# Performance work log

Measured on AMD Instinct MI355X. Metric: run time of the kernel, lower is better.

The kernel has to match this reference:

```python
import jax, jax.numpy as jnp
import numpy as np

N_NODES = 100000
N_EDGES = 1000000
IN_DIM = 64
OUT_DIM = 64
BN_EPS = 1e-5


def setup_inputs() -> dict:
    key = jax.random.key(0)
    k1, k2, k3 = jax.random.split(key, 3)
    x = jax.random.normal(k1, (N_NODES, IN_DIM), dtype=jnp.float32)
    edge_index = jax.random.randint(k2, (2, N_EDGES), 0, N_NODES, dtype=jnp.int32)
    W = jax.random.normal(k3, (IN_DIM, OUT_DIM), dtype=jnp.float32) * (1.0 / np.sqrt(IN_DIM))
    b = jnp.zeros((OUT_DIM,), dtype=jnp.float32)
    gamma = jnp.ones((OUT_DIM,), dtype=jnp.float32)
    beta = jnp.zeros((OUT_DIM,), dtype=jnp.float32)
    return {"x": x, "edge_index": edge_index, "W": W, "b": b, "gamma": gamma, "beta": beta}


def reference(x, edge_index, W, b, gamma, beta):
    N = x.shape[0]
    # GCN normalization with self-loops (improved=False -> fill value 1.0)
    loop = jnp.arange(N, dtype=edge_index.dtype)
    src = jnp.concatenate([edge_index[0], loop])  # message sources
    dst = jnp.concatenate([edge_index[1], loop])  # aggregation targets
    ew = jnp.ones(src.shape[0], dtype=x.dtype)
    deg = jax.ops.segment_sum(ew, dst, num_segments=N)  # [N]
    dinv = jnp.where(deg > 0, jax.lax.rsqrt(deg), 0.0)
    norm = dinv[src] * ew * dinv[dst]  # [E+N]
    # linear transform then normalized scatter-add aggregation
    h = x @ W  # [N, OUT_DIM]
    msg = h[src] * norm[:, None]  # [E+N, OUT_DIM]
    agg = jax.ops.segment_sum(msg, dst, num_segments=N) + b  # [N, OUT_DIM]
    # activation
    a = jax.nn.relu(agg)
    # BatchNorm1d, training mode: batch statistics over node dim (biased var)
    mean = jnp.mean(a, axis=0)
    var = jnp.mean((a - mean) ** 2, axis=0)
    out = gamma * (a - mean) * jax.lax.rsqrt(var + BN_EPS) + beta
    return out
```

## Files before the change

kernel.cpp:

```cpp
#include <hip/hip_runtime.h>
#include <hip/hip_fp16.h>

#define DIM 64
#define BN_EPS 1e-5f
#define RSHIFT 8
#define RSIZE 256
#define EPB 2048
#define ABLK 2048
#define RBLK 128
#define BH 512

__global__ __launch_bounds__(256) void k_binhist(const int* __restrict__ dst,
                                                 int* __restrict__ bhist,
                                                 int P, int E) {
    __shared__ int hist[BH];
    for (int b0 = threadIdx.x; b0 < BH; b0 += 256) hist[b0] = 0;
    __syncthreads();
    const int base4 = blockIdx.x * (EPB / 4);
    for (int i = 0; i < EPB / 4 / 256; ++i) {
        int idx = base4 + i * 256 + threadIdx.x;
        int e0 = idx << 2;
        if (e0 + 3 < E) {
            int4 d4 = ((const int4*)dst)[idx];
            atomicAdd(&hist[d4.x >> RSHIFT], 1);
            atomicAdd(&hist[d4.y >> RSHIFT], 1);
            atomicAdd(&hist[d4.z >> RSHIFT], 1);
            atomicAdd(&hist[d4.w >> RSHIFT], 1);
        } else {
            for (int k = 0; k < 4; ++k)
                if (e0 + k < E) atomicAdd(&hist[dst[e0 + k] >> RSHIFT], 1);
        }
    }
    __syncthreads();
    for (int b0 = threadIdx.x; b0 < P; b0 += 256)
        bhist[blockIdx.x * BH + b0] = hist[b0];
}

__global__ __launch_bounds__(128) void k_binscan(int* __restrict__ bhist,
                                                 int* __restrict__ bintot,
                                                 int nbin) {
    __shared__ int s[128];
    const int r = blockIdx.x;
    int carry = 0;
    for (int base = 0; base < nbin; base += 128) {
        const int idx = base + threadIdx.x;
        int v = (idx < nbin) ? bhist[idx * BH + r] : 0;
        s[threadIdx.x] = v;
        __syncthreads();
        for (int off = 1; off < 128; off <<= 1) {
            int t = (threadIdx.x >= (unsigned)off) ? s[threadIdx.x - off] : 0;
            __syncthreads();
            s[threadIdx.x] += t;
            __syncthreads();
        }
        if (idx < nbin) bhist[idx * BH + r] = carry + s[threadIdx.x] - v;
        carry += s[127];
        __syncthreads();
    }
    if (threadIdx.x == 0) bintot[r] = carry;
}

__global__ void k_gscan(const int* __restrict__ bintot, int* __restrict__ gbase,
                        int* __restrict__ rowptr, int P, int N, int E) {
    __shared__ int s[512];
    int v = ((int)threadIdx.x < P) ? bintot[threadIdx.x] : 0;
    s[threadIdx.x] = v;
    __syncthreads();
    for (int off = 1; off < 512; off <<= 1) {
        int t = (threadIdx.x >= (unsigned)off) ? s[threadIdx.x - off] : 0;
        __syncthreads();
        s[threadIdx.x] += t;
        __syncthreads();
    }
    if ((int)threadIdx.x < P) gbase[threadIdx.x] = s[threadIdx.x] - v;
    if ((int)threadIdx.x == P - 1) gbase[P] = s[threadIdx.x];
    if (threadIdx.x == 0) rowptr[N] = E;
}

__global__ __launch_bounds__(256) void k_bin(const int* __restrict__ src,
                                             const int* __restrict__ dst,
                                             const int* __restrict__ gbase,
                                             const int* __restrict__ bhist,
                                             int* __restrict__ pk, int P, int E) {
    __shared__ int gofs[BH], lcnt[BH];
    for (int b0 = threadIdx.x; b0 < P; b0 += 256) {
        gofs[b0] = gbase[b0] + bhist[blockIdx.x * BH + b0];
        lcnt[b0] = 0;
    }
    __syncthreads();
    const int base4 = blockIdx.x * (EPB / 4);
    for (int i = 0; i < EPB / 4 / 256; ++i) {
        int idx = base4 + i * 256 + threadIdx.x;
        int e0 = idx << 2;
        if (e0 + 3 < E) {
            int4 d4 = ((const int4*)dst)[idx];
            int4 s4 = ((const int4*)src)[idx];
            int b0;
            b0 = d4.x >> RSHIFT; pk[gofs[b0] + atomicAdd(&lcnt[b0], 1)] = ((d4.x & (RSIZE - 1)) << 20) | s4.x;
            b0 = d4.y >> RSHIFT; pk[gofs[b0] + atomicAdd(&lcnt[b0], 1)] = ((d4.y & (RSIZE - 1)) << 20) | s4.y;
            b0 = d4.z >> RSHIFT; pk[gofs[b0] + atomicAdd(&lcnt[b0], 1)] = ((d4.z & (RSIZE - 1)) << 20) | s4.z;
            b0 = d4.w >> RSHIFT; pk[gofs[b0] + atomicAdd(&lcnt[b0], 1)] = ((d4.w & (RSIZE - 1)) << 20) | s4.w;
        } else {
            for (int k = 0; k < 4; ++k) {
                if (e0 + k < E) {
                    int d = dst[e0 + k];
                    int b0 = d >> RSHIFT;
                    pk[gofs[b0] + atomicAdd(&lcnt[b0], 1)] = ((d & (RSIZE - 1)) << 20) | src[e0 + k];
                }
            }
        }
    }
}

__global__ __launch_bounds__(512) void k_sortrange(
        const int* __restrict__ gbase, const int* __restrict__ pk,
        int* __restrict__ ssrc, int* __restrict__ rowptr,
        float* __restrict__ dinv, int N) {
    __shared__ int lhist[256], ls[256], lcur[256];
    const int r = blockIdx.x;
    const int d0 = r << RSHIFT;
    const int tid = threadIdx.x;
    const int i = d0 + tid;
    const int ebeg = gbase[r], eend = gbase[r + 1];
    if (tid < 256) lhist[tid] = 0;
    __syncthreads();
    for (int j = ebeg + tid; j < eend; j += 512)
        atomicAdd(&lhist[((unsigned)pk[j]) >> 20], 1);
    __syncthreads();
    int dg = 0;
    if (tid < 256) {
        dg = lhist[tid];
        if (i < N) dinv[i] = rsqrtf((float)dg + 1.0f);
        ls[tid] = dg;
    }
    __syncthreads();
    for (int off = 1; off < 256; off <<= 1) {
        int t = (tid < 256 && tid >= off) ? ls[tid - off] : 0;
        __syncthreads();
        if (tid < 256) ls[tid] += t;
        __syncthreads();
    }
    if (tid < 256) {
        int lofs = ls[tid] - dg;
        lcur[tid] = ebeg + lofs;
        if (i < N) rowptr[i] = ebeg + lofs;
    }
    __syncthreads();
    for (int j = ebeg + tid; j < eend; j += 512) {
        int p = pk[j];
        ssrc[atomicAdd(&lcur[((unsigned)p) >> 20], 1)] = p & 0xFFFFF;
    }
}

__global__ __launch_bounds__(256) void k_gemm(const float* __restrict__ x,
                                              const float* __restrict__ W,
                                              const float* __restrict__ dinv,
                                              __half* __restrict__ h2, int N) {
    __shared__ float Wl[DIM * DIM];
    for (int i = threadIdx.x; i < DIM * DIM; i += 256) Wl[i] = W[i];
    __syncthreads();
    int t = blockIdx.x * 256 + threadIdx.x;
    int r = t >> 2;
    int q = t & 3;
    if (r >= N) return;
    const float4* xr4 = (const float4*)(x + (size_t)r * DIM);
    float4 acc[4];
#pragma unroll
    for (int j = 0; j < 4; ++j) acc[j] = make_float4(0.f, 0.f, 0.f, 0.f);
    for (int k0 = 0; k0 < 16; ++k0) {
        float4 xv = xr4[k0];
#pragma unroll
        for (int kk = 0; kk < 4; ++kk) {
            float xs = (&xv.x)[kk];
            const float4* wrow = (const float4*)(Wl + (k0 * 4 + kk) * DIM) + (q << 2);
#pragma unroll
            for (int j = 0; j < 4; ++j) {
                float4 w = wrow[j];
                acc[j].x += xs * w.x;
                acc[j].y += xs * w.y;
                acc[j].z += xs * w.z;
                acc[j].w += xs * w.w;
            }
        }
    }
    float dr = dinv[r];
    float4* hr4 = (float4*)(h2 + (size_t)r * DIM) + (q << 1);
    union { __half2 h[4]; float4 f4; } pack;
#pragma unroll
    for (int j = 0; j < 4; j += 2) {
        pack.h[0] = __float22half2_rn(make_float2(acc[j].x * dr, acc[j].y * dr));
        pack.h[1] = __float22half2_rn(make_float2(acc[j].z * dr, acc[j].w * dr));
        pack.h[2] = __float22half2_rn(make_float2(acc[j + 1].x * dr, acc[j + 1].y * dr));
        pack.h[3] = __float22half2_rn(make_float2(acc[j + 1].z * dr, acc[j + 1].w * dr));
        hr4[j >> 1] = pack.f4;
    }
}

#define GATHER_BATCH(B)                                                             \
    {                                                                               \
        int sA[B]; float vA[B];                                                     \
        _Pragma("unroll")                                                           \
        for (int k = 0; k < B; ++k) sA[k] = __builtin_amdgcn_readlane(sv, j + k);   \
        _Pragma("unroll")                                                           \
        for (int k = 0; k < B; ++k) vA[k] = __half2float(hb[(size_t)sA[k] * DIM]);  \
        _Pragma("unroll")                                                           \
        for (int k = 0; k < B; ++k) {                                               \
            if (j + k < c) acc0 += vA[k]; else acc1 += vA[k];                       \
        }                                                                           \
        j += B;                                                                     \
    }

__global__ __launch_bounds__(256) void k_nodeagg(
        const int* __restrict__ rowptr, const int* __restrict__ ssrc,
        const __half* __restrict__ h2, const float* __restrict__ dinv,
        const float* __restrict__ b, __half* __restrict__ a2,
        float* __restrict__ pstats, int N) {
    const int lane = threadIdx.x & 63;
    const int w = threadIdx.x >> 6;
    const float bl = b[lane];
    const __half* hb = h2 + lane;
    float psum = 0.f, psq = 0.f;
    const int npairs = N >> 1;
    for (int t = blockIdx.x * 4 + w; t < npairs; t += ABLK * 4) {
        const int i0 = t << 1;
        const int rb0 = rowptr[i0], rb1 = rowptr[i0 + 1], rb2 = rowptr[i0 + 2];
        float acc0 = __half2float(hb[(size_t)i0 * DIM]);
        float acc1 = __half2float(hb[(size_t)(i0 + 1) * DIM]);
        const int total = rb2 - rb0;
        for (int j0 = 0; j0 < total; j0 += 64) {
            const int m = min(64, total - j0);
            const int c = rb1 - rb0 - j0;
            int sv = ssrc[rb0 + j0 + min(lane, m - 1)];
            int j = 0;
            while (j + 16 <= m) GATHER_BATCH(16)
            if (j + 8 <= m) GATHER_BATCH(8)
            if (j + 4 <= m) GATHER_BATCH(4)
            for (; j < m; ++j) {
                int sj = __builtin_amdgcn_readlane(sv, j);
                float v = __half2float(hb[(size_t)sj * DIM]);
                if (j < c) acc0 += v; else acc1 += v;
            }
        }
        float a0 = fmaxf(acc0 * dinv[i0] + bl, 0.f);
        float a1 = fmaxf(acc1 * dinv[i0 + 1] + bl, 0.f);
        a2[(size_t)i0 * DIM + lane] = __float2half_rn(a0);
        a2[(size_t)(i0 + 1) * DIM + lane] = __float2half_rn(a1);
        psum += a0 + a1;
        psq += a0 * a0 + a1 * a1;
    }
    __shared__ float s1[256], s2[256];
    s1[threadIdx.x] = psum;
    s2[threadIdx.x] = psq;
    __syncthreads();
    if (threadIdx.x < 128) {
        s1[threadIdx.x] += s1[threadIdx.x + 128];
        s2[threadIdx.x] += s2[threadIdx.x + 128];
    }
    __syncthreads();
    if (threadIdx.x < 64) {
        pstats[(size_t)blockIdx.x * 128 + threadIdx.x] = s1[threadIdx.x] + s1[threadIdx.x + 64];
        pstats[(size_t)blockIdx.x * 128 + 64 + threadIdx.x] = s2[threadIdx.x] + s2[threadIdx.x + 64];
    }
}

__global__ __launch_bounds__(128) void k_redstats(const float* __restrict__ pstats,
                                                  float* __restrict__ pstats2) {
    const int f = threadIdx.x;
    const size_t base = (size_t)blockIdx.x * (ABLK / RBLK) * 128;
    float s = 0.f;
#pragma unroll 8
    for (int j = 0; j < ABLK / RBLK; ++j)
        s += pstats[base + (size_t)j * 128 + f];
    pstats2[(size_t)blockIdx.x * 128 + f] = s;
}

__global__ void k_finstats(const float* __restrict__ pstats2,
                           const float* __restrict__ gamma, const float* __restrict__ beta,
                           float* __restrict__ scale, float* __restrict__ shift, int N) {
    __shared__ float ssum[1024], ssq[1024];
    const int f = threadIdx.x & 63;
    const int c = threadIdx.x >> 6;
    float s = 0.f, q = 0.f;
    for (int blk = c; blk < RBLK; blk += 16) {
        s += pstats2[blk * 128 + f];
        q += pstats2[blk * 128 + 64 + f];
    }
    ssum[threadIdx.x] = s;
    ssq[threadIdx.x] = q;
    __syncthreads();
    for (int o = 512; o >= 64; o >>= 1) {
        if ((int)threadIdx.x < o) {
            ssum[threadIdx.x] += ssum[threadIdx.x + o];
            ssq[threadIdx.x] += ssq[threadIdx.x + o];
        }
        __syncthreads();
    }
    if (threadIdx.x < 64) {
        float inv_n = 1.0f / (float)N;
        float mean = ssum[f] * inv_n;
        float var = ssq[f] * inv_n - mean * mean;
        float istd = rsqrtf(var + BN_EPS);
        float sc = gamma[f] * istd;
        scale[f] = sc;
        shift[f] = beta[f] - mean * sc;
    }
}

__global__ void k_bn2(const __half* __restrict__ a2, const float* __restrict__ scale,
                      const float* __restrict__ shift, float* __restrict__ out, int total8) {
    int i = blockIdx.x * blockDim.x + threadIdx.x;
    const int stride = gridDim.x * blockDim.x;
    const int f8 = i & 7;
    const float4 sc0 = ((const float4*)scale)[f8 * 2];
    const float4 sc1 = ((const float4*)scale)[f8 * 2 + 1];
    const float4 sh0 = ((const float4*)shift)[f8 * 2];
    const float4 sh1 = ((const float4*)shift)[f8 * 2 + 1];
    for (; i < total8; i += stride) {
        union { float4 f; __half2 h[4]; } u;
        u.f = ((const float4*)a2)[i];
        float2 p0 = __half22float2(u.h[0]);
        float2 p1 = __half22float2(u.h[1]);
        float2 p2 = __half22float2(u.h[2]);
        float2 p3 = __half22float2(u.h[3]);
        float4 o0 = make_float4(p0.x * sc0.x + sh0.x, p0.y * sc0.y + sh0.y,
                                p1.x * sc0.z + sh0.z, p1.y * sc0.w + sh0.w);
        float4 o1 = make_float4(p2.x * sc1.x + sh1.x, p2.y * sc1.y + sh1.y,
                                p3.x * sc1.z + sh1.z, p3.y * sc1.w + sh1.w);
        ((float4*)out)[(size_t)i * 2] = o0;
        ((float4*)out)[(size_t)i * 2 + 1] = o1;
    }
}

extern "C" void kernel_launch(void* const* d_in, const int* in_sizes, int n_in,
                              void* d_out, int out_size, void* d_ws, size_t ws_size,
                              hipStream_t stream) {
    const float* x     = (const float*)d_in[0];
    const int*   ei    = (const int*)d_in[1];
    const float* W     = (const float*)d_in[2];
    const float* b     = (const float*)d_in[3];
    const float* gamma = (const float*)d_in[4];
    const float* beta  = (const float*)d_in[5];
    float* out = (float*)d_out;

    const int N = in_sizes[0] / DIM;
    const int E = in_sizes[1] / 2;
    const int* esrc = ei;
    const int* edst = ei + E;
    const int P = (N + RSIZE - 1) >> RSHIFT;
    const int nbin = (E + EPB - 1) / EPB;

    char* ws = (char*)d_ws;
    size_t off = 0;
    int* bhist = (int*)(ws + off);      off += (size_t)nbin * BH * sizeof(int);
    off = (off + 255) & ~(size_t)255;
    int* bintot = (int*)(ws + off);     off += 512 * sizeof(int);
    int* gbase = (int*)(ws + off);      off += 520 * sizeof(int);
    off = (off + 255) & ~(size_t)255;
    float* dinv = (float*)(ws + off);   off += (size_t)N * sizeof(float);
    off = (off + 255) & ~(size_t)255;
    int* rowptr = (int*)(ws + off);     off += (size_t)(N + 1) * sizeof(int);
    off = (off + 255) & ~(size_t)255;
    float* scale = (float*)(ws + off);  off += 64 * sizeof(float);
    float* shift = (float*)(ws + off);  off += 64 * sizeof(float);
    off = (off + 255) & ~(size_t)255;
    float* pstats = (float*)(ws + off); off += (size_t)ABLK * 128 * sizeof(float);
    off = (off + 255) & ~(size_t)255;
    float* pstats2 = (float*)(ws + off); off += (size_t)RBLK * 128 * sizeof(float);
    off = (off + 255) & ~(size_t)255;
    int* pk = (int*)(ws + off);         off += (size_t)E * sizeof(int);
    off = (off + 255) & ~(size_t)255;
    int* ssrc = (int*)(ws + off);       off += (size_t)E * sizeof(int);
    off = (off + 255) & ~(size_t)255;
    __half* h2 = (__half*)(ws + off);   off += (size_t)N * DIM * sizeof(__half);
    off = (off + 255) & ~(size_t)255;
    __half* a2 = (__half*)(ws + off);   off += (size_t)N * DIM * sizeof(__half);

    k_binhist<<<nbin, 256, 0, stream>>>(edst, bhist, P, E);
    k_binscan<<<P, 128, 0, stream>>>(bhist, bintot, nbin);
    k_gscan<<<1, 512, 0, stream>>>(bintot, gbase, rowptr, P, N, E);
    k_bin<<<nbin, 256, 0, stream>>>(esrc, edst, gbase, bhist, pk, P, E);
    k_sortrange<<<P, 512, 0, stream>>>(gbase, pk, ssrc, rowptr, dinv, N);
    k_gemm<<<(4 * N + 255) / 256, 256, 0, stream>>>(x, W, dinv, h2, N);
    k_nodeagg<<<ABLK, 256, 0, stream>>>(rowptr, ssrc, h2, dinv, b, a2, pstats, N);
    k_redstats<<<RBLK, 128, 0, stream>>>(pstats, pstats2);
    k_finstats<<<1, 1024, 0, stream>>>(pstats2, gamma, beta, scale, shift, N);
    k_bn2<<<1024, 256, 0, stream>>>(a2, scale, shift, out, N * DIM / 8);
}
```

Baseline: 181.5 us.

## Fuse histogram and binning into one pass with block-local bucketed output

The two-pass global bucket sort (histogram, scan, then scatter) becomes a single kernel in which each block histograms its 2048 edges, scans locally, and writes packed entries grouped by bucket into its own slice of the pk buffer. Per-block offsets and counts are packed into one metadata word. The binscan is replaced by a plain reduction, and sortrange now walks every block's segment for its bucket. This drops one full read of the edge arrays and one kernel launch. In exchange, sortrange does irregular, serial per-thread loops over many small segments (about 489 blocks per bucket, with only a few entries each), which may load-balance and coalesce poorly.

```diff
diff --git a/kernel.cpp b/kernel.cpp
--- a/kernel.cpp
+++ b/kernel.cpp
@@ -10,54 +10,64 @@
 #define RBLK 128
 #define BH 512
 
-__global__ __launch_bounds__(256) void k_binhist(const int* __restrict__ dst,
-                                                 int* __restrict__ bhist,
-                                                 int P, int E) {
-    __shared__ int hist[BH];
-    for (int b0 = threadIdx.x; b0 < BH; b0 += 256) hist[b0] = 0;
-    __syncthreads();
-    const int base4 = blockIdx.x * (EPB / 4);
-    for (int i = 0; i < EPB / 4 / 256; ++i) {
-        int idx = base4 + i * 256 + threadIdx.x;
-        int e0 = idx << 2;
-        if (e0 + 3 < E) {
-            int4 d4 = ((const int4*)dst)[idx];
-            atomicAdd(&hist[d4.x >> RSHIFT], 1);
-            atomicAdd(&hist[d4.y >> RSHIFT], 1);
-            atomicAdd(&hist[d4.z >> RSHIFT], 1);
-            atomicAdd(&hist[d4.w >> RSHIFT], 1);
-        } else {
-            for (int k = 0; k < 4; ++k)
-                if (e0 + k < E) atomicAdd(&hist[dst[e0 + k] >> RSHIFT], 1);
-        }
-    }
-    __syncthreads();
-    for (int b0 = threadIdx.x; b0 < P; b0 += 256)
-        bhist[blockIdx.x * BH + b0] = hist[b0];
-}
-
-__global__ __launch_bounds__(128) void k_binscan(int* __restrict__ bhist,
-                                                 int* __restrict__ bintot,
-                                                 int nbin) {
+__global__ __launch_bounds__(512) void k_bin2(const int* __restrict__ src,
+                                              const int* __restrict__ dst,
+                                              int* __restrict__ meta,
+                                              int* __restrict__ pk, int P, int E) {
+    __shared__ int hist[BH], ls[BH], lcur[BH];
+    const int tid = threadIdx.x;
+    hist[tid] = 0;
+    __syncthreads();
+    const int idx = blockIdx.x * 512 + tid;
+    const int e0 = idx << 2;
+    int d[4], s[4];
+    int vc = 0;
+    if (e0 + 3 < E) {
+        int4 d4 = ((const int4*)dst)[idx];
+        int4 s4 = ((const int4*)src)[idx];
+        d[0] = d4.x; d[1] = d4.y; d[2] = d4.z; d[3] = d4.w;
+        s[0] = s4.x; s[1] = s4.y; s[2] = s4.z; s[3] = s4.w;
+        vc = 4;
+    } else {
+        for (int k = 0; k < 4; ++k)
+            if (e0 + k < E) { d[vc] = dst[e0 + k]; s[vc] = src[e0 + k]; ++vc; }
+    }
+    for (int k = 0; k < vc; ++k) atomicAdd(&hist[d[k] >> RSHIFT], 1);
+    __syncthreads();
+    int cnt = hist[tid];
+    ls[tid] = cnt;
+    __syncthreads();
+    for (int off = 1; off < 512; off <<= 1) {
+        int t = (tid >= off) ? ls[tid - off] : 0;
+        __syncthreads();
+        ls[tid] += t;
+        __syncthreads();
+    }
+    int lofs = ls[tid] - cnt;
+    lcur[tid] = lofs;
+    if (tid < P) meta[blockIdx.x * BH + tid] = (lofs << 12) | cnt;
+    __syncthreads();
+    const int base = blockIdx.x * EPB;
+    for (int k = 0; k < vc; ++k) {
+        int b = d[k] >> RSHIFT;
+        pk[base + atomicAdd(&lcur[b], 1)] = ((d[k] & (RSIZE - 1)) << 20) | s[k];
+    }
+}
+
+__global__ __launch_bounds__(128) void k_binred(const int* __restrict__ meta,
+                                                int* __restrict__ bintot, int nbin) {
     __shared__ int s[128];
     const int r = blockIdx.x;
-    int carry = 0;
-    for (int base = 0; base < nbin; base += 128) {
-        const int idx = base + threadIdx.x;
-        int v = (idx < nbin) ? bhist[idx * BH + r] : 0;
-        s[threadIdx.x] = v;
-        __syncthreads();
-        for (int off = 1; off < 128; off <<= 1) {
-            int t = (threadIdx.x >= (unsigned)off) ? s[threadIdx.x - off] : 0;
-            __syncthreads();
-            s[threadIdx.x] += t;
-            __syncthreads();
-        }
-        if (idx < nbin) bhist[idx * BH + r] = carry + s[threadIdx.x] - v;
-        carry += s[127];
-        __syncthreads();
-    }
-    if (threadIdx.x == 0) bintot[r] = carry;
+    int acc = 0;
+    for (int idx = threadIdx.x; idx < nbin; idx += 128)
+        acc += meta[idx * BH + r] & 0xFFF;
+    s[threadIdx.x] = acc;
+    __syncthreads();
+    for (int o = 64; o > 0; o >>= 1) {
+        if ((int)threadIdx.x < o) s[threadIdx.x] += s[threadIdx.x + o];
+        __syncthreads();
+    }
+    if (threadIdx.x == 0) bintot[r] = s[0];
 }
 
 __global__ void k_gscan(const int* __restrict__ bintot, int* __restrict__ gbase,
@@ -77,59 +87,29 @@
     if (threadIdx.x == 0) rowptr[N] = E;
 }
 
-__global__ __launch_bounds__(256) void k_bin(const int* __restrict__ src,
-                                             const int* __restrict__ dst,
-                                             const int* __restrict__ gbase,
-                                             const int* __restrict__ bhist,
-                                             int* __restrict__ pk, int P, int E) {
-    __shared__ int gofs[BH], lcnt[BH];
-    for (int b0 = threadIdx.x; b0 < P; b0 += 256) {
-        gofs[b0] = gbase[b0] + bhist[blockIdx.x * BH + b0];
-        lcnt[b0] = 0;
-    }
-    __syncthreads();
-    const int base4 = blockIdx.x * (EPB / 4);
-    for (int i = 0; i < EPB / 4 / 256; ++i) {
-        int idx = base4 + i * 256 + threadIdx.x;
-        int e0 = idx << 2;
-        if (e0 + 3 < E) {
-            int4 d4 = ((const int4*)dst)[idx];
-            int4 s4 = ((const int4*)src)[idx];
-            int b0;
-            b0 = d4.x >> RSHIFT; pk[gofs[b0] + atomicAdd(&lcnt[b0], 1)] = ((d4.x & (RSIZE - 1)) << 20) | s4.x;
-            b0 = d4.y >> RSHIFT; pk[gofs[b0] + atomicAdd(&lcnt[b0], 1)] = ((d4.y & (RSIZE - 1)) << 20) | s4.y;
-            b0 = d4.z >> RSHIFT; pk[gofs[b0] + atomicAdd(&lcnt[b0], 1)] = ((d4.z & (RSIZE - 1)) << 20) | s4.z;
-            b0 = d4.w >> RSHIFT; pk[gofs[b0] + atomicAdd(&lcnt[b0], 1)] = ((d4.w & (RSIZE - 1)) << 20) | s4.w;
-        } else {
-            for (int k = 0; k < 4; ++k) {
-                if (e0 + k < E) {
-                    int d = dst[e0 + k];
-                    int b0 = d >> RSHIFT;
-                    pk[gofs[b0] + atomicAdd(&lcnt[b0], 1)] = ((d & (RSIZE - 1)) << 20) | src[e0 + k];
-                }
-            }
-        }
-    }
-}
-
 __global__ __launch_bounds__(512) void k_sortrange(
-        const int* __restrict__ gbase, const int* __restrict__ pk,
-        int* __restrict__ ssrc, int* __restrict__ rowptr,
-        float* __restrict__ dinv, int N) {
+        const int* __restrict__ gbase, const int* __restrict__ meta,
+        const int* __restrict__ pk, int* __restrict__ ssrc,
+        int* __restrict__ rowptr, float* __restrict__ dinv, int N, int nbin) {
     __shared__ int lhist[256], ls[256], lcur[256];
     const int r = blockIdx.x;
     const int d0 = r << RSHIFT;
     const int tid = threadIdx.x;
-    const int i = d0 + tid;
-    const int ebeg = gbase[r], eend = gbase[r + 1];
+    const int ebeg = gbase[r];
     if (tid < 256) lhist[tid] = 0;
     __syncthreads();
-    for (int j = ebeg + tid; j < eend; j += 512)
-        atomicAdd(&lhist[((unsigned)pk[j]) >> 20], 1);
+    for (int blk = tid; blk < nbin; blk += 512) {
+        int m = meta[blk * BH + r];
+        int cnt = m & 0xFFF, lofs = (m >> 12) & 0xFFF;
+        const int* p = pk + blk * EPB + lofs;
+        for (int i = 0; i < cnt; ++i)
+            atomicAdd(&lhist[((unsigned)p[i]) >> 20], 1);
+    }
     __syncthreads();
     int dg = 0;
     if (tid < 256) {
         dg = lhist[tid];
+        int i = d0 + tid;
         if (i < N) dinv[i] = rsqrtf((float)dg + 1.0f);
         ls[tid] = dg;
     }
@@ -143,12 +123,18 @@
     if (tid < 256) {
         int lofs = ls[tid] - dg;
         lcur[tid] = ebeg + lofs;
+        int i = d0 + tid;
         if (i < N) rowptr[i] = ebeg + lofs;
     }
     __syncthreads();
-    for (int j = ebeg + tid; j < eend; j += 512) {
-        int p = pk[j];
-        ssrc[atomicAdd(&lcur[((unsigned)p) >> 20], 1)] = p & 0xFFFFF;
+    for (int blk = tid; blk < nbin; blk += 512) {
+        int m = meta[blk * BH + r];
+        int cnt = m & 0xFFF, lofs = (m >> 12) & 0xFFF;
+        const int* p = pk + blk * EPB + lofs;
+        for (int i = 0; i < cnt; ++i) {
+            int v = p[i];
+            ssrc[atomicAdd(&lcur[((unsigned)v) >> 20], 1)] = v & 0xFFFFF;
+        }
     }
 }
 
@@ -351,7 +337,7 @@
 
     char* ws = (char*)d_ws;
     size_t off = 0;
-    int* bhist = (int*)(ws + off);      off += (size_t)nbin * BH * sizeof(int);
+    int* meta = (int*)(ws + off);       off += (size_t)nbin * BH * sizeof(int);
     off = (off + 255) & ~(size_t)255;
     int* bintot = (int*)(ws + off);     off += 512 * sizeof(int);
     int* gbase = (int*)(ws + off);      off += 520 * sizeof(int);
@@ -367,7 +353,7 @@
     off = (off + 255) & ~(size_t)255;
     float* pstats2 = (float*)(ws + off); off += (size_t)RBLK * 128 * sizeof(float);
     off = (off + 255) & ~(size_t)255;
-    int* pk = (int*)(ws + off);         off += (size_t)E * sizeof(int);
+    int* pk = (int*)(ws + off);         off += (size_t)nbin * EPB * sizeof(int);
     off = (off + 255) & ~(size_t)255;
     int* ssrc = (int*)(ws + off);       off += (size_t)E * sizeof(int);
     off = (off + 255) & ~(size_t)255;
@@ -375,11 +361,10 @@
     off = (off + 255) & ~(size_t)255;
     __half* a2 = (__half*)(ws + off);   off += (size_t)N * DIM * sizeof(__half);
 
-    k_binhist<<<nbin, 256, 0, stream>>>(edst, bhist, P, E);
-    k_binscan<<<P, 128, 0, stream>>>(bhist, bintot, nbin);
+    k_bin2<<<nbin, 512, 0, stream>>>(esrc, edst, meta, pk, P, E);
+    k_binred<<<P, 128, 0, stream>>>(meta, bintot, nbin);
     k_gscan<<<1, 512, 0, stream>>>(bintot, gbase, rowptr, P, N, E);
-    k_bin<<<nbin, 256, 0, stream>>>(esrc, edst, gbase, bhist, pk, P, E);
-    k_sortrange<<<P, 512, 0, stream>>>(gbase, pk, ssrc, rowptr, dinv, N);
+    k_sortrange<<<P, 512, 0, stream>>>(gbase, meta, pk, ssrc, rowptr, dinv, N, nbin);
     k_gemm<<<(4 * N + 255) / 256, 256, 0, stream>>>(x, W, dinv, h2, N);
     k_nodeagg<<<ABLK, 256, 0, stream>>>(rowptr, ssrc, h2, dinv, b, a2, pstats, N);
     k_redstats<<<RBLK, 128, 0, stream>>>(pstats, pstats2);
```

After: 185.5 us. +2.2%, slower.

## Fuse GEMM with edge histogram kernel and apply source dinv during gather

Applied to the files above, without the earlier changes.

The GEMM no longer scales rows by dinv, which removes its dependence on the degree computation. It can then be merged into the first histogram kernel as extra blocks of one launch, so the dense transform overlaps with the edge binning and one launch is saved. In exchange, the aggregation kernel now loads dinv[src] for every gathered edge, adding one scattered 4-byte load per edge on top of the half-precision feature gather.

```diff
diff --git a/kernel.cpp b/kernel.cpp
--- a/kernel.cpp
+++ b/kernel.cpp
@@ -10,30 +10,71 @@
 #define RBLK 128
 #define BH 512
 
-__global__ __launch_bounds__(256) void k_binhist(const int* __restrict__ dst,
-                                                 int* __restrict__ bhist,
-                                                 int P, int E) {
-    __shared__ int hist[BH];
-    for (int b0 = threadIdx.x; b0 < BH; b0 += 256) hist[b0] = 0;
-    __syncthreads();
-    const int base4 = blockIdx.x * (EPB / 4);
-    for (int i = 0; i < EPB / 4 / 256; ++i) {
-        int idx = base4 + i * 256 + threadIdx.x;
-        int e0 = idx << 2;
-        if (e0 + 3 < E) {
-            int4 d4 = ((const int4*)dst)[idx];
-            atomicAdd(&hist[d4.x >> RSHIFT], 1);
-            atomicAdd(&hist[d4.y >> RSHIFT], 1);
-            atomicAdd(&hist[d4.z >> RSHIFT], 1);
-            atomicAdd(&hist[d4.w >> RSHIFT], 1);
-        } else {
-            for (int k = 0; k < 4; ++k)
-                if (e0 + k < E) atomicAdd(&hist[dst[e0 + k] >> RSHIFT], 1);
-        }
-    }
-    __syncthreads();
-    for (int b0 = threadIdx.x; b0 < P; b0 += 256)
-        bhist[blockIdx.x * BH + b0] = hist[b0];
+__global__ __launch_bounds__(256) void k_hist_gemm(
+        const int* __restrict__ dst, int* __restrict__ bhist,
+        const float* __restrict__ x, const float* __restrict__ W,
+        __half* __restrict__ h2, int P, int E, int nbin, int N) {
+    if ((int)blockIdx.x < nbin) {
+        __shared__ int hist[BH];
+        for (int b0 = threadIdx.x; b0 < BH; b0 += 256) hist[b0] = 0;
+        __syncthreads();
+        const int base4 = blockIdx.x * (EPB / 4);
+        for (int i = 0; i < EPB / 4 / 256; ++i) {
+            int idx = base4 + i * 256 + threadIdx.x;
+            int e0 = idx << 2;
+            if (e0 + 3 < E) {
+                int4 d4 = ((const int4*)dst)[idx];
+                atomicAdd(&hist[d4.x >> RSHIFT], 1);
+                atomicAdd(&hist[d4.y >> RSHIFT], 1);
+                atomicAdd(&hist[d4.z >> RSHIFT], 1);
+                atomicAdd(&hist[d4.w >> RSHIFT], 1);
+            } else {
+                for (int k = 0; k < 4; ++k)
+                    if (e0 + k < E) atomicAdd(&hist[dst[e0 + k] >> RSHIFT], 1);
+            }
+        }
+        __syncthreads();
+        for (int b0 = threadIdx.x; b0 < P; b0 += 256)
+            bhist[blockIdx.x * BH + b0] = hist[b0];
+    } else {
+        __shared__ float Wl[DIM * DIM];
+        for (int i = threadIdx.x; i < DIM * DIM; i += 256) Wl[i] = W[i];
+        __syncthreads();
+        int t = ((int)blockIdx.x - nbin) * 256 + threadIdx.x;
+        int r = t >> 2;
+        int q = t & 3;
+        if (r >= N) return;
+        const float4* xr4 = (const float4*)(x + (size_t)r * DIM);
+        float4 acc[4];
+#pragma unroll
+        for (int j = 0; j < 4; ++j) acc[j] = make_float4(0.f, 0.f, 0.f, 0.f);
+        for (int k0 = 0; k0 < 16; ++k0) {
+            float4 xv = xr4[k0];
+#pragma unroll
+            for (int kk = 0; kk < 4; ++kk) {
+                float xs = (&xv.x)[kk];
+                const float4* wrow = (const float4*)(Wl + (k0 * 4 + kk) * DIM) + (q << 2);
+#pragma unroll
+                for (int j = 0; j < 4; ++j) {
+                    float4 w = wrow[j];
+                    acc[j].x += xs * w.x;
+                    acc[j].y += xs * w.y;
+                    acc[j].z += xs * w.z;
+                    acc[j].w += xs * w.w;
+                }
+            }
+        }
+        float4* hr4 = (float4*)(h2 + (size_t)r * DIM) + (q << 1);
+        union { __half2 h[4]; float4 f4; } pack;
+#pragma unroll
+        for (int j = 0; j < 4; j += 2) {
+            pack.h[0] = __float22half2_rn(make_float2(acc[j].x, acc[j].y));
+            pack.h[1] = __float22half2_rn(make_float2(acc[j].z, acc[j].w));
+            pack.h[2] = __float22half2_rn(make_float2(acc[j + 1].x, acc[j + 1].y));
+            pack.h[3] = __float22half2_rn(make_float2(acc[j + 1].z, acc[j + 1].w));
+            hr4[j >> 1] = pack.f4;
+        }
+    }
 }
 
 __global__ __launch_bounds__(128) void k_binscan(int* __restrict__ bhist,
@@ -152,60 +193,18 @@
     }
 }
 
-__global__ __launch_bounds__(256) void k_gemm(const float* __restrict__ x,
-                                              const float* __restrict__ W,
-                                              const float* __restrict__ dinv,
-                                              __half* __restrict__ h2, int N) {
-    __shared__ float Wl[DIM * DIM];
-    for (int i = threadIdx.x; i < DIM * DIM; i += 256) Wl[i] = W[i];
-    __syncthreads();
-    int t = blockIdx.x * 256 + threadIdx.x;
-    int r = t >> 2;
-    int q = t & 3;
-    if (r >= N) return;
-    const float4* xr4 = (const float4*)(x + (size_t)r * DIM);
-    float4 acc[4];
-#pragma unroll
-    for (int j = 0; j < 4; ++j) acc[j] = make_float4(0.f, 0.f, 0.f, 0.f);
-    for (int k0 = 0; k0 < 16; ++k0) {
-        float4 xv = xr4[k0];
-#pragma unroll
-        for (int kk = 0; kk < 4; ++kk) {
-            float xs = (&xv.x)[kk];
-            const float4* wrow = (const float4*)(Wl + (k0 * 4 + kk) * DIM) + (q << 2);
-#pragma unroll
-            for (int j = 0; j < 4; ++j) {
-                float4 w = wrow[j];
-                acc[j].x += xs * w.x;
-                acc[j].y += xs * w.y;
-                acc[j].z += xs * w.z;
-                acc[j].w += xs * w.w;
-            }
-        }
-    }
-    float dr = dinv[r];
-    float4* hr4 = (float4*)(h2 + (size_t)r * DIM) + (q << 1);
-    union { __half2 h[4]; float4 f4; } pack;
-#pragma unroll
-    for (int j = 0; j < 4; j += 2) {
-        pack.h[0] = __float22half2_rn(make_float2(acc[j].x * dr, acc[j].y * dr));
-        pack.h[1] = __float22half2_rn(make_float2(acc[j].z * dr, acc[j].w * dr));
-        pack.h[2] = __float22half2_rn(make_float2(acc[j + 1].x * dr, acc[j + 1].y * dr));
-        pack.h[3] = __float22half2_rn(make_float2(acc[j + 1].z * dr, acc[j + 1].w * dr));
-        hr4[j >> 1] = pack.f4;
-    }
-}
-
 #define GATHER_BATCH(B)                                                             \
     {                                                                               \
-        int sA[B]; float vA[B];                                                     \
+        int sA[B]; float vA[B]; float dA[B];                                        \
         _Pragma("unroll")                                                           \
         for (int k = 0; k < B; ++k) sA[k] = __builtin_amdgcn_readlane(sv, j + k);   \
         _Pragma("unroll")                                                           \
         for (int k = 0; k < B; ++k) vA[k] = __half2float(hb[(size_t)sA[k] * DIM]);  \
         _Pragma("unroll")                                                           \
+        for (int k = 0; k < B; ++k) dA[k] = dinv[sA[k]];                            \
+        _Pragma("unroll")                                                           \
         for (int k = 0; k < B; ++k) {                                               \
-            if (j + k < c) acc0 += vA[k]; else acc1 += vA[k];                       \
+            if (j + k < c) acc0 += vA[k] * dA[k]; else acc1 += vA[k] * dA[k];       \
         }                                                                           \
         j += B;                                                                     \
     }
@@ -224,8 +223,9 @@
     for (int t = blockIdx.x * 4 + w; t < npairs; t += ABLK * 4) {
         const int i0 = t << 1;
         const int rb0 = rowptr[i0], rb1 = rowptr[i0 + 1], rb2 = rowptr[i0 + 2];
-        float acc0 = __half2float(hb[(size_t)i0 * DIM]);
-        float acc1 = __half2float(hb[(size_t)(i0 + 1) * DIM]);
+        const float dv0 = dinv[i0], dv1 = dinv[i0 + 1];
+        float acc0 = __half2float(hb[(size_t)i0 * DIM]) * dv0;
+        float acc1 = __half2float(hb[(size_t)(i0 + 1) * DIM]) * dv1;
         const int total = rb2 - rb0;
         for (int j0 = 0; j0 < total; j0 += 64) {
             const int m = min(64, total - j0);
@@ -237,12 +237,12 @@
             if (j + 4 <= m) GATHER_BATCH(4)
             for (; j < m; ++j) {
                 int sj = __builtin_amdgcn_readlane(sv, j);
-                float v = __half2float(hb[(size_t)sj * DIM]);
+                float v = __half2float(hb[(size_t)sj * DIM]) * dinv[sj];
                 if (j < c) acc0 += v; else acc1 += v;
             }
         }
-        float a0 = fmaxf(acc0 * dinv[i0] + bl, 0.f);
-        float a1 = fmaxf(acc1 * dinv[i0 + 1] + bl, 0.f);
+        float a0 = fmaxf(acc0 * dv0 + bl, 0.f);
+        float a1 = fmaxf(acc1 * dv1 + bl, 0.f);
         a2[(size_t)i0 * DIM + lane] = __float2half_rn(a0);
         a2[(size_t)(i0 + 1) * DIM + lane] = __float2half_rn(a1);
         psum += a0 + a1;
@@ -348,6 +348,7 @@
     const int* edst = ei + E;
     const int P = (N + RSIZE - 1) >> RSHIFT;
     const int nbin = (E + EPB - 1) / EPB;
+    const int gemmblocks = (4 * N + 255) / 256;
 
     char* ws = (char*)d_ws;
     size_t off = 0;
@@ -375,12 +376,11 @@
     off = (off + 255) & ~(size_t)255;
     __half* a2 = (__half*)(ws + off);   off += (size_t)N * DIM * sizeof(__half);
 
-    k_binhist<<<nbin, 256, 0, stream>>>(edst, bhist, P, E);
+    k_hist_gemm<<<nbin + gemmblocks, 256, 0, stream>>>(edst, bhist, x, W, h2, P, E, nbin, N);
     k_binscan<<<P, 128, 0, stream>>>(bhist, bintot, nbin);
     k_gscan<<<1, 512, 0, stream>>>(bintot, gbase, rowptr, P, N, E);
     k_bin<<<nbin, 256, 0, stream>>>(esrc, edst, gbase, bhist, pk, P, E);
     k_sortrange<<<P, 512, 0, stream>>>(gbase, pk, ssrc, rowptr, dinv, N);
-    k_gemm<<<(4 * N + 255) / 256, 256, 0, stream>>>(x, W, dinv, h2, N);
     k_nodeagg<<<ABLK, 256, 0, stream>>>(rowptr, ssrc, h2, dinv, b, a2, pstats, N);
     k_redstats<<<RBLK, 128, 0, stream>>>(pstats, pstats2);
     k_finstats<<<1, 1024, 0, stream>>>(pstats2, gamma, beta, scale, shift, N);
```

Measured after the change: 182.8 us. Within noise of the previous version (+0.7%).
